# Kernel tuning notes

Hardware: AMD Instinct MI355X
Metric: run time of the kernel (lower is better)

The kernel has to match this reference:

```python
import jax, jax.numpy as jnp
import numpy as np

B, L, D, H = 2, 256, 512, 8
DH = D // H
EPS = 1e-12
NEG = -1000000000000000.0


def setup_inputs() -> dict:
    key = jax.random.key(0)
    ks = jax.random.split(key, 16)
    s = 0.02
    return {
        "inputs": jax.random.normal(ks[0], (B, L, D), jnp.float32),
        "pos_embedding": jax.random.normal(ks[1], (B, L, L, D), jnp.float32),
        "seq_mask": jnp.ones((B, L), jnp.int32),
        "Wq": jax.random.normal(ks[2], (D, D), jnp.float32) * s,
        "bq": jnp.zeros((D,), jnp.float32),
        "Wk": jax.random.normal(ks[3], (D, D), jnp.float32) * s,
        "bk": jnp.zeros((D,), jnp.float32),
        "Wv": jax.random.normal(ks[4], (D, D), jnp.float32) * s,
        "bv": jnp.zeros((D,), jnp.float32),
        "Wr": jax.random.normal(ks[5], (D, D), jnp.float32) * s,
        "br": jnp.zeros((D,), jnp.float32),
        "u": jax.random.normal(ks[6], (H, DH), jnp.float32),
        "v": jax.random.normal(ks[7], (H, DH), jnp.float32),
        "Wf": jax.random.normal(ks[8], (D, D), jnp.float32) * s,
        "bf": jnp.zeros((D,), jnp.float32),
        "gamma": jnp.ones((D,), jnp.float32),
        "beta": jnp.zeros((D,), jnp.float32),
    }


def _layer_norm(x, gamma, beta, eps):
    mu = jnp.mean(x, axis=-1, keepdims=True)
    var = jnp.mean(jnp.square(x - mu), axis=-1, keepdims=True)
    return (x - mu) * jax.lax.rsqrt(var + eps) * gamma + beta


def reference(inputs, pos_embedding, seq_mask, Wq, bq, Wk, bk, Wv, bv, Wr, br,
              u, v, Wf, bf, gamma, beta):
    b, l, d = inputs.shape
    # projections (nn.Linear: x @ W.T + b)
    q = (inputs @ Wq.T + bq).reshape(b, l, H, DH).transpose(0, 2, 1, 3)  # [B,H,L,DH]
    k = (inputs @ Wk.T + bk).reshape(b, l, H, DH).transpose(0, 2, 1, 3)
    vv = (inputs @ Wv.T + bv).reshape(b, l, H, DH).transpose(0, 2, 1, 3)
    rel = (pos_embedding @ Wr.T + br).reshape(b, l, l, H, DH)            # [B,L,L,H,DH]

    # A + C: content-content + content-bias
    A_C = jnp.einsum('bhid,bhjd->bhij', q + u[None, :, None, :], k)
    # B + D: position term against per-(i,j) relative embeddings
    B_D = jnp.einsum('bhid,bijhd->bhij', q + v[None, :, None, :], rel)

    score = (A_C + B_D) / np.sqrt(DH).astype(np.float32)
    invalid = (seq_mask == 0)[:, None, None, :]   # mask keys where seq_mask==0
    score = jnp.where(invalid, NEG, score)
    attn = jax.nn.softmax(score, axis=-1)

    ctx = jnp.einsum('bhij,bhjd->bhid', attn, vv)
    ctx = ctx.transpose(0, 2, 1, 3).reshape(b, l, d)

    # FFN (single dense) + residual + LayerNorm
    h = ctx @ Wf.T + bf
    return _layer_norm(h + inputs, gamma, beta, EPS)
```

## Files before the change

### kernel.cpp

```cpp
#include <hip/hip_runtime.h>
#include <cmath>


typedef __bf16 bf16x8 __attribute__((ext_vector_type(8)));
typedef float f32x4 __attribute__((ext_vector_type(4)));

__device__ __forceinline__ float4 ld4(const float* p) { return *reinterpret_cast<const float4*>(p); }
__device__ __forceinline__ void st4(float* p, float4 v) { *reinterpret_cast<float4*>(p) = v; }
__device__ __forceinline__ void fma4(float4& a, float s, const float4& v) {
    a.x = fmaf(s, v.x, a.x); a.y = fmaf(s, v.y, a.y);
    a.z = fmaf(s, v.z, a.z); a.w = fmaf(s, v.w, a.w);
}
__device__ __forceinline__ float dot4(const float4& a, const float4& b) {
    return a.x*b.x + a.y*b.y + a.z*b.z + a.w*b.w;
}
__device__ __forceinline__ unsigned short f2bf(float f) {
    unsigned int x = __float_as_uint(f);
    unsigned int r = x + 0x7FFFu + ((x >> 16) & 1u);
    return (unsigned short)(r >> 16);
}
__device__ __forceinline__ ushort4 cvt4u(float4 a) {
    ushort4 u;
    u.x = f2bf(a.x); u.y = f2bf(a.y); u.z = f2bf(a.z); u.w = f2bf(a.w);
    return u;
}
__device__ __forceinline__ bf16x8 cvt8(float4 a, float4 b) {
    bf16x8 r;
    r[0] = (__bf16)a.x; r[1] = (__bf16)a.y; r[2] = (__bf16)a.z; r[3] = (__bf16)a.w;
    r[4] = (__bf16)b.x; r[5] = (__bf16)b.y; r[6] = (__bf16)b.z; r[7] = (__bf16)b.w;
    return r;
}

__device__ __forceinline__ void mfma_tile(
        const float* __restrict__ Abase, int ldA,
        const float* __restrict__ Bbase, int ldB,
        int K, int lane, f32x4 acc[4]) {
    int koff = (lane >> 4) * 8;
    int rr = lane & 15;
    const float* ap = Abase + rr * ldA + koff;
    const float* bp = Bbase + rr * ldB + koff;
#pragma unroll 2
    for (int k0 = 0; k0 < K; k0 += 32) {
        float4 a0  = ld4(ap + k0),            a1  = ld4(ap + k0 + 4);
        float4 b00 = ld4(bp + k0),            b01 = ld4(bp + k0 + 4);
        float4 b10 = ld4(bp + 16*ldB + k0),   b11 = ld4(bp + 16*ldB + k0 + 4);
        float4 b20 = ld4(bp + 32*ldB + k0),   b21 = ld4(bp + 32*ldB + k0 + 4);
        float4 b30 = ld4(bp + 48*ldB + k0),   b31 = ld4(bp + 48*ldB + k0 + 4);
        bf16x8 af = cvt8(a0, a1);
        acc[0] = __builtin_amdgcn_mfma_f32_16x16x32_bf16(af, cvt8(b00, b01), acc[0], 0, 0, 0);
        acc[1] = __builtin_amdgcn_mfma_f32_16x16x32_bf16(af, cvt8(b10, b11), acc[1], 0, 0, 0);
        acc[2] = __builtin_amdgcn_mfma_f32_16x16x32_bf16(af, cvt8(b20, b21), acc[2], 0, 0, 0);
        acc[3] = __builtin_amdgcn_mfma_f32_16x16x32_bf16(af, cvt8(b30, b31), acc[3], 0, 0, 0);
    }
}

__global__ __launch_bounds__(256) void k_front(
        const float* __restrict__ x,
        const float* __restrict__ Wq, const float* __restrict__ Wk, const float* __restrict__ Wv,
        const float* __restrict__ bq, const float* __restrict__ bk, const float* __restrict__ bv,
        const float* __restrict__ Wr,
        const float* __restrict__ u, const float* __restrict__ vbv, const float* __restrict__ br,
        float* __restrict__ qw, float* __restrict__ kw, float* __restrict__ vw,
        float* __restrict__ wrt,
        float* __restrict__ c_ws, float* __restrict__ uk_ws, float* __restrict__ vwr_ws) {
    int id = blockIdx.x;
    int t = threadIdx.x;
    if (id < 192) {
        int mat = id >> 6, rem = id & 63;
        int m0 = (rem >> 3) * 64, n0 = (rem & 7) * 64;
        const float* W   = (mat == 0) ? Wq : (mat == 1) ? Wk : Wv;
        const float* bias= (mat == 0) ? bq : (mat == 1) ? bk : bv;
        float* out       = (mat == 0) ? qw : (mat == 1) ? kw : vw;
        int wv = t >> 6, lane = t & 63;
        f32x4 acc[4] = {{0,0,0,0},{0,0,0,0},{0,0,0,0},{0,0,0,0}};
        mfma_tile(x + (m0 + wv * 16) * 512, 512, W + n0 * 512, 512, 512, lane, acc);
        int h = n0 >> 6;
        int col = lane & 15, rbase = (lane >> 4) * 4;
        float rpart[4] = {0, 0, 0, 0};
#pragma unroll
        for (int c = 0; c < 4; c++) {
            int d = c * 16 + col;
            float bv_ = bias[n0 + d];
            float vbd = vbv[n0 + d];
            float brd = br[n0 + d];
            float ud  = u[n0 + d];
#pragma unroll
            for (int r = 0; r < 4; r++) {
                int m = m0 + wv * 16 + rbase + r;
                int b = m >> 8, i = m & 255;
                float val = acc[c][r] + bv_;
                out[((b * 8 + h) * 256 + i) * 64 + d] = val;
                if (mat == 0) rpart[r] += (val + vbd) * brd;
                else if (mat == 1) rpart[r] += val * ud;
            }
        }
        if (mat < 2) {
#pragma unroll
            for (int msk = 1; msk < 16; msk <<= 1) {
#pragma unroll
                for (int r = 0; r < 4; r++) rpart[r] += __shfl_xor(rpart[r], msk, 64);
            }
            if (col == 0) {
                float* dst = (mat == 0) ? c_ws : uk_ws;
#pragma unroll
                for (int r = 0; r < 4; r++) {
                    int m = m0 + wv * 16 + rbase + r;
                    int b = m >> 8, i = m & 255;
                    dst[(b * 8 + h) * 256 + i] = rpart[r];
                }
            }
        }
    } else {
        __shared__ float tile[64][65];
        __shared__ float vpart[4][64];
        int id2 = id - 192;
        int n0 = (id2 >> 3) * 64, k0 = (id2 & 7) * 64;
        int h = n0 >> 6;
        int tx = t & 63, ty = t >> 6;
#pragma unroll
        for (int r = 0; r < 16; r++) {
            int row = ty * 16 + r;
            tile[row][tx] = Wr[(n0 + row) * 512 + k0 + tx];
        }
        __syncthreads();
#pragma unroll
        for (int r = 0; r < 16; r++) {
            int row = ty * 16 + r;
            wrt[(k0 + row) * 512 + n0 + tx] = tile[tx][row];
        }
        float s = 0.f;
#pragma unroll
        for (int r = 0; r < 16; r++) s += vbv[n0 + ty * 16 + r] * tile[ty * 16 + r][tx];
        vpart[ty][tx] = s;
        __syncthreads();
        if (t < 64) vwr_ws[h * 512 + k0 + t] = vpart[0][t] + vpart[1][t] + vpart[2][t] + vpart[3][t];
    }
}

__global__ __launch_bounds__(256) void k_mid(
        const float* __restrict__ qw, const float* __restrict__ kw,
        const float* __restrict__ wrt,
        const float* __restrict__ c_ws, const float* __restrict__ uk_ws,
        const float* __restrict__ vwr_ws,
        float* __restrict__ w_ws, float* __restrict__ ac_ws) {
    int id = blockIdx.x;
    int t = threadIdx.x, wv = t >> 6, lane = t & 63;
    int col = lane & 15, rbase = (lane >> 4) * 4;
    if (id < 512) {
        int h = id >> 6, rem = id & 63;
        int m0 = (rem >> 3) * 64, n0 = (rem & 7) * 64;
        int b = m0 >> 8, i0 = m0 & 255;
        f32x4 acc[4] = {{0,0,0,0},{0,0,0,0},{0,0,0,0},{0,0,0,0}};
        mfma_tile(qw + ((b * 8 + h) * 256 + i0 + wv * 16) * 64, 64,
                  wrt + (size_t)n0 * 512 + h * 64, 512, 64, lane, acc);
#pragma unroll
        for (int c = 0; c < 4; c++) {
            int n = n0 + c * 16 + col;
            float vw_ = vwr_ws[h * 512 + n];
#pragma unroll
            for (int r = 0; r < 4; r++) {
                int m = m0 + wv * 16 + rbase + r;
                w_ws[((size_t)m * 8 + h) * 512 + n] = acc[c][r] + vw_;
            }
        }
    } else {
        int id2 = id - 512;
        int bh = id2 >> 4, rem2 = id2 & 15;
        int b = bh >> 3, h = bh & 7;
        int i0 = (rem2 >> 2) * 64, j0 = (rem2 & 3) * 64;
        f32x4 acc[4] = {{0,0,0,0},{0,0,0,0},{0,0,0,0},{0,0,0,0}};
        mfma_tile(qw + ((b * 8 + h) * 256 + i0 + wv * 16) * 64, 64,
                  kw + ((b * 8 + h) * 256 + j0) * 64, 64, 64, lane, acc);
#pragma unroll
        for (int c = 0; c < 4; c++) {
            int j = j0 + c * 16 + col;
            float ukv = uk_ws[(b * 8 + h) * 256 + j];
#pragma unroll
            for (int r = 0; r < 4; r++) {
                int ii = i0 + wv * 16 + rbase + r;
                float ci = c_ws[(b * 8 + h) * 256 + ii];
                ac_ws[((size_t)(b * 256 + ii) * 8 + h) * 256 + j] = acc[c][r] + ukv + ci;
            }
        }
    }
}

__global__ __launch_bounds__(512, 4) void k_attn(
        const float* __restrict__ pos, const float* __restrict__ w_ws,
        const float* __restrict__ ac_ws, const float* __restrict__ vw,
        const int* __restrict__ seq_mask, float* __restrict__ ctx) {
    int bi = blockIdx.x;
    int b = bi >> 8, i = bi & 255;
    int t = threadIdx.x;
    int wv = t >> 6, lane = t & 63;
    __shared__ unsigned short wl[16 * 512];
    __shared__ float sc[8][256];
    __shared__ unsigned short stage[8][2048];

    {
        int h = t >> 6;
        int j = t & 63;
        const float* src = w_ws + ((size_t)bi * 8 + h) * 512 + j * 8;
        float4 a = ld4(src);
        float4 c = ld4(src + 4);
        char* dst = reinterpret_cast<char*>(wl) + (j >> 2) * 1024 + ((j & 3) * 16 + h) * 16;
        *reinterpret_cast<ushort4*>(dst)     = cvt4u(a);
        *reinterpret_cast<ushort4*>(dst + 8) = cvt4u(c);
    }
    __syncthreads();

    const float* pb = pos + (size_t)bi * (256 * 512);
    int jbase = wv * 32;
    char* sb = reinterpret_cast<char*>(&stage[wv][0]);
    int arow = lane & 15;
    int a_off = arow * 256 + (lane >> 4) * 16;
    int b_off = (lane & 15) * 16 + (lane >> 4) * 256;
    const char* wlc = reinterpret_cast<const char*>(wl);

#pragma unroll
    for (int jt = 0; jt < 2; jt++) {
        f32x4 acc = {0, 0, 0, 0};
#pragma unroll
        for (int eh = 0; eh < 4; eh++) {
            const float* src = pb + (size_t)(jbase + jt * 16 + (lane >> 5)) * 512
                             + eh * 128 + (lane & 31) * 4;
            float4 tmp[8];
#pragma unroll
            for (int s = 0; s < 8; s++) tmp[s] = ld4(src + (size_t)s * 2 * 512);
#pragma unroll
            for (int s = 0; s < 8; s++) {
                int row = (lane >> 5) + s * 2;
                *reinterpret_cast<ushort4*>(sb + row * 256 + (lane & 31) * 8) = cvt4u(tmp[s]);
            }
#pragma unroll
            for (int es = 0; es < 4; es++) {
                bf16x8 af = *reinterpret_cast<const bf16x8*>(sb + a_off + es * 64);
                int estep = eh * 4 + es;
                bf16x8 bf = *reinterpret_cast<const bf16x8*>(wlc + estep * 1024 + b_off);
                acc = __builtin_amdgcn_mfma_f32_16x16x32_bf16(af, bf, acc, 0, 0, 0);
            }
        }
        int h = lane & 15;
        int rbase = (lane >> 4) * 4;
        if (h < 8) {
#pragma unroll
            for (int r = 0; r < 4; r++) sc[h][jbase + jt * 16 + rbase + r] = acc[r];
        }
    }
    __syncthreads();

    {
        int h = wv;
        const float* acrow = ac_ws + ((b * 256 + i) * 8 + h) * 256;
        float vals[4];
        float mx = -INFINITY;
#pragma unroll
        for (int r = 0; r < 4; r++) {
            int j = lane + r * 64;
            float s = (sc[h][j] + acrow[j]) * 0.125f;
            if (seq_mask[b * 256 + j] == 0) s = -1e15f;
            vals[r] = s;
            mx = fmaxf(mx, s);
        }
#pragma unroll
        for (int m = 32; m >= 1; m >>= 1) mx = fmaxf(mx, __shfl_xor(mx, m, 64));
        float sum = 0.f;
#pragma unroll
        for (int r = 0; r < 4; r++) { vals[r] = __expf(vals[r] - mx); sum += vals[r]; }
#pragma unroll
        for (int m = 32; m >= 1; m >>= 1) sum += __shfl_xor(sum, m, 64);
        float inv = 1.0f / sum;
#pragma unroll
        for (int r = 0; r < 4; r++) sc[h][lane + r * 64] = vals[r] * inv;
    }

    float4* part = reinterpret_cast<float4*>(&stage[0][0]);
    {
        int h = wv;
        int d4 = (lane & 15) * 4;
        int js = lane >> 4;
        const float* vbase = vw + (size_t)(b * 8 + h) * 256 * 64 + d4;
        float4 acc = {0, 0, 0, 0};
#pragma unroll 2
        for (int r = 0; r < 64; r += 4) {
            int j = js * 64 + r;
            float p0 = sc[h][j + 0], p1 = sc[h][j + 1];
            float p2 = sc[h][j + 2], p3 = sc[h][j + 3];
            float4 v0 = ld4(vbase + (size_t)(j + 0) * 64);
            float4 v1 = ld4(vbase + (size_t)(j + 1) * 64);
            float4 v2 = ld4(vbase + (size_t)(j + 2) * 64);
            float4 v3 = ld4(vbase + (size_t)(j + 3) * 64);
            fma4(acc, p0, v0); fma4(acc, p1, v1);
            fma4(acc, p2, v2); fma4(acc, p3, v3);
        }
        part[(h * 4 + js) * 16 + (lane & 15)] = acc;
    }
    {
        int h = wv;
        if ((lane >> 4) == 0) {
            int l = lane & 15;
            float4 a0 = part[(h * 4 + 0) * 16 + l], a1 = part[(h * 4 + 1) * 16 + l];
            float4 a2 = part[(h * 4 + 2) * 16 + l], a3 = part[(h * 4 + 3) * 16 + l];
            float4 o;
            o.x = a0.x + a1.x + a2.x + a3.x;
            o.y = a0.y + a1.y + a2.y + a3.y;
            o.z = a0.z + a1.z + a2.z + a3.z;
            o.w = a0.w + a1.w + a2.w + a3.w;
            st4(ctx + (size_t)(b * 256 + i) * 512 + h * 64 + l * 4, o);
        }
    }
}

__global__ __launch_bounds__(256) void k_ffn(
        const float* __restrict__ A, const float* __restrict__ Wf,
        const float* __restrict__ bias, const float* __restrict__ resid,
        float* __restrict__ outp) {
    int m0 = blockIdx.x * 64, n0 = blockIdx.y * 64;
    int t = threadIdx.x, wv = t >> 6, lane = t & 63;
    f32x4 acc[4] = {{0,0,0,0},{0,0,0,0},{0,0,0,0},{0,0,0,0}};
    mfma_tile(A + (m0 + wv * 16) * 512, 512, Wf + n0 * 512, 512, 512, lane, acc);
    int col = lane & 15, rbase = (lane >> 4) * 4;
#pragma unroll
    for (int c = 0; c < 4; c++) {
        int n = n0 + c * 16 + col;
        float bv_ = bias[n];
#pragma unroll
        for (int r = 0; r < 4; r++) {
            int m = m0 + wv * 16 + rbase + r;
            outp[m * 512 + n] = acc[c][r] + bv_ + resid[m * 512 + n];
        }
    }
}

__global__ __launch_bounds__(256) void k_ln(
        const float* __restrict__ tmp, const float* __restrict__ gamma,
        const float* __restrict__ beta, float* __restrict__ out) {
    int m = blockIdx.x, t = threadIdx.x;
    int wv = t >> 6, lane = t & 63;
    float2 xv = *reinterpret_cast<const float2*>(&tmp[m * 512 + t * 2]);
    __shared__ float red[4];
    float s = xv.x + xv.y;
#pragma unroll
    for (int k = 32; k >= 1; k >>= 1) s += __shfl_xor(s, k, 64);
    if (lane == 0) red[wv] = s;
    __syncthreads();
    float mu = (red[0] + red[1] + red[2] + red[3]) * (1.0f / 512.0f);
    __syncthreads();
    float dx = xv.x - mu, dy = xv.y - mu;
    float vs = dx * dx + dy * dy;
#pragma unroll
    for (int k = 32; k >= 1; k >>= 1) vs += __shfl_xor(vs, k, 64);
    if (lane == 0) red[wv] = vs;
    __syncthreads();
    float var = (red[0] + red[1] + red[2] + red[3]) * (1.0f / 512.0f);
    float rstd = rsqrtf(var + 1e-12f);
    float2 g = *reinterpret_cast<const float2*>(&gamma[t * 2]);
    float2 be = *reinterpret_cast<const float2*>(&beta[t * 2]);
    float2 o;
    o.x = dx * rstd * g.x + be.x;
    o.y = dy * rstd * g.y + be.y;
    *reinterpret_cast<float2*>(&out[m * 512 + t * 2]) = o;
}

extern "C" void kernel_launch(void* const* d_in, const int* in_sizes, int n_in,
                              void* d_out, int out_size, void* d_ws, size_t ws_size,
                              hipStream_t stream) {
    const float* x     = (const float*)d_in[0];
    const float* pos   = (const float*)d_in[1];
    const int*   smask = (const int*)d_in[2];
    const float* Wq = (const float*)d_in[3];
    const float* bq = (const float*)d_in[4];
    const float* Wk = (const float*)d_in[5];
    const float* bk = (const float*)d_in[6];
    const float* Wv = (const float*)d_in[7];
    const float* bv = (const float*)d_in[8];
    const float* Wr = (const float*)d_in[9];
    const float* br = (const float*)d_in[10];
    const float* u  = (const float*)d_in[11];
    const float* vb = (const float*)d_in[12];
    const float* Wf = (const float*)d_in[13];
    const float* bf = (const float*)d_in[14];
    const float* gamma = (const float*)d_in[15];
    const float* beta  = (const float*)d_in[16];
    float* out = (float*)d_out;

    float* ws = (float*)d_ws;
    float* q_ws   = ws;
    float* k_ws   = q_ws  + 262144;
    float* v_ws   = k_ws  + 262144;
    float* w_ws   = v_ws  + 262144;
    float* ac_ws  = w_ws  + 2097152;
    float* ctx_ws = ac_ws + 1048576;
    float* tmp_ws = ctx_ws + 262144;
    float* wrt_ws = tmp_ws + 262144;
    float* c_ws   = wrt_ws + 262144;
    float* uk_ws  = c_ws  + 4096;
    float* vwr_ws = uk_ws + 4096;

    k_front<<<dim3(256), 256, 0, stream>>>(x, Wq, Wk, Wv, bq, bk, bv, Wr, u, vb, br,
                                           q_ws, k_ws, v_ws, wrt_ws, c_ws, uk_ws, vwr_ws);
    k_mid<<<dim3(768), 256, 0, stream>>>(q_ws, k_ws, wrt_ws, c_ws, uk_ws, vwr_ws, w_ws, ac_ws);
    k_attn<<<dim3(512), 512, 0, stream>>>(pos, w_ws, ac_ws, v_ws, smask, ctx_ws);
    k_ffn<<<dim3(8, 8), 256, 0, stream>>>(ctx_ws, Wf, bf, x, tmp_ws);
    k_ln<<<dim3(512), 256, 0, stream>>>(tmp_ws, gamma, beta, out);
}
```

Measured before the change: 108.1 us.

## Fuse output projection, residual and LayerNorm into attention kernel epilogue

```diff
diff --git a/kernel.cpp b/kernel.cpp
--- a/kernel.cpp
+++ b/kernel.cpp
@@ -58,10 +58,10 @@
         const float* __restrict__ x,
         const float* __restrict__ Wq, const float* __restrict__ Wk, const float* __restrict__ Wv,
         const float* __restrict__ bq, const float* __restrict__ bk, const float* __restrict__ bv,
-        const float* __restrict__ Wr,
+        const float* __restrict__ Wr, const float* __restrict__ Wf,
         const float* __restrict__ u, const float* __restrict__ vbv, const float* __restrict__ br,
         float* __restrict__ qw, float* __restrict__ kw, float* __restrict__ vw,
-        float* __restrict__ wrt,
+        float* __restrict__ wrt, float* __restrict__ wft,
         float* __restrict__ c_ws, float* __restrict__ uk_ws, float* __restrict__ vwr_ws) {
     int id = blockIdx.x;
     int t = threadIdx.x;
@@ -113,27 +113,32 @@
     } else {
         __shared__ float tile[64][65];
         __shared__ float vpart[4][64];
-        int id2 = id - 192;
+        int isWf = (id >= 256);
+        int id2 = id - (isWf ? 256 : 192);
+        const float* Wsrc = isWf ? Wf : Wr;
+        float* Wdst = isWf ? wft : wrt;
         int n0 = (id2 >> 3) * 64, k0 = (id2 & 7) * 64;
         int h = n0 >> 6;
         int tx = t & 63, ty = t >> 6;
 #pragma unroll
         for (int r = 0; r < 16; r++) {
             int row = ty * 16 + r;
-            tile[row][tx] = Wr[(n0 + row) * 512 + k0 + tx];
+            tile[row][tx] = Wsrc[(n0 + row) * 512 + k0 + tx];
         }
         __syncthreads();
 #pragma unroll
         for (int r = 0; r < 16; r++) {
             int row = ty * 16 + r;
-            wrt[(k0 + row) * 512 + n0 + tx] = tile[tx][row];
-        }
-        float s = 0.f;
-#pragma unroll
-        for (int r = 0; r < 16; r++) s += vbv[n0 + ty * 16 + r] * tile[ty * 16 + r][tx];
-        vpart[ty][tx] = s;
-        __syncthreads();
-        if (t < 64) vwr_ws[h * 512 + k0 + t] = vpart[0][t] + vpart[1][t] + vpart[2][t] + vpart[3][t];
+            Wdst[(k0 + row) * 512 + n0 + tx] = tile[tx][row];
+        }
+        if (!isWf) {
+            float s = 0.f;
+#pragma unroll
+            for (int r = 0; r < 16; r++) s += vbv[n0 + ty * 16 + r] * tile[ty * 16 + r][tx];
+            vpart[ty][tx] = s;
+            __syncthreads();
+            if (t < 64) vwr_ws[h * 512 + k0 + t] = vpart[0][t] + vpart[1][t] + vpart[2][t] + vpart[3][t];
+        }
     }
 }
 
@@ -188,7 +193,11 @@
 __global__ __launch_bounds__(512, 4) void k_attn(
         const float* __restrict__ pos, const float* __restrict__ w_ws,
         const float* __restrict__ ac_ws, const float* __restrict__ vw,
-        const int* __restrict__ seq_mask, float* __restrict__ ctx) {
+        const int* __restrict__ seq_mask,
+        const float* __restrict__ wft, const float* __restrict__ bf,
+        const float* __restrict__ x,
+        const float* __restrict__ gamma, const float* __restrict__ beta,
+        float* __restrict__ outp) {
     int bi = blockIdx.x;
     int b = bi >> 8, i = bi & 255;
     int t = threadIdx.x;
@@ -196,6 +205,8 @@
     __shared__ unsigned short wl[16 * 512];
     __shared__ float sc[8][256];
     __shared__ unsigned short stage[8][2048];
+    __shared__ float ctxl[512];
+    __shared__ float lnred[8][2];
 
     {
         int h = t >> 6;
@@ -236,8 +247,8 @@
             for (int es = 0; es < 4; es++) {
                 bf16x8 af = *reinterpret_cast<const bf16x8*>(sb + a_off + es * 64);
                 int estep = eh * 4 + es;
-                bf16x8 bf = *reinterpret_cast<const bf16x8*>(wlc + estep * 1024 + b_off);
-                acc = __builtin_amdgcn_mfma_f32_16x16x32_bf16(af, bf, acc, 0, 0, 0);
+                bf16x8 bf_ = *reinterpret_cast<const bf16x8*>(wlc + estep * 1024 + b_off);
+                acc = __builtin_amdgcn_mfma_f32_16x16x32_bf16(af, bf_, acc, 0, 0, 0);
             }
         }
         int h = lane & 15;
@@ -306,60 +317,45 @@
             o.y = a0.y + a1.y + a2.y + a3.y;
             o.z = a0.z + a1.z + a2.z + a3.z;
             o.w = a0.w + a1.w + a2.w + a3.w;
-            st4(ctx + (size_t)(b * 256 + i) * 512 + h * 64 + l * 4, o);
-        }
-    }
-}
-
-__global__ __launch_bounds__(256) void k_ffn(
-        const float* __restrict__ A, const float* __restrict__ Wf,
-        const float* __restrict__ bias, const float* __restrict__ resid,
-        float* __restrict__ outp) {
-    int m0 = blockIdx.x * 64, n0 = blockIdx.y * 64;
-    int t = threadIdx.x, wv = t >> 6, lane = t & 63;
-    f32x4 acc[4] = {{0,0,0,0},{0,0,0,0},{0,0,0,0},{0,0,0,0}};
-    mfma_tile(A + (m0 + wv * 16) * 512, 512, Wf + n0 * 512, 512, 512, lane, acc);
-    int col = lane & 15, rbase = (lane >> 4) * 4;
-#pragma unroll
-    for (int c = 0; c < 4; c++) {
-        int n = n0 + c * 16 + col;
-        float bv_ = bias[n];
-#pragma unroll
-        for (int r = 0; r < 4; r++) {
-            int m = m0 + wv * 16 + rbase + r;
-            outp[m * 512 + n] = acc[c][r] + bv_ + resid[m * 512 + n];
-        }
-    }
-}
-
-__global__ __launch_bounds__(256) void k_ln(
-        const float* __restrict__ tmp, const float* __restrict__ gamma,
-        const float* __restrict__ beta, float* __restrict__ out) {
-    int m = blockIdx.x, t = threadIdx.x;
-    int wv = t >> 6, lane = t & 63;
-    float2 xv = *reinterpret_cast<const float2*>(&tmp[m * 512 + t * 2]);
-    __shared__ float red[4];
-    float s = xv.x + xv.y;
-#pragma unroll
-    for (int k = 32; k >= 1; k >>= 1) s += __shfl_xor(s, k, 64);
-    if (lane == 0) red[wv] = s;
+            st4(&ctxl[h * 64 + l * 4], o);
+        }
+    }
     __syncthreads();
-    float mu = (red[0] + red[1] + red[2] + red[3]) * (1.0f / 512.0f);
-    __syncthreads();
-    float dx = xv.x - mu, dy = xv.y - mu;
-    float vs = dx * dx + dy * dy;
-#pragma unroll
-    for (int k = 32; k >= 1; k >>= 1) vs += __shfl_xor(vs, k, 64);
-    if (lane == 0) red[wv] = vs;
-    __syncthreads();
-    float var = (red[0] + red[1] + red[2] + red[3]) * (1.0f / 512.0f);
-    float rstd = rsqrtf(var + 1e-12f);
-    float2 g = *reinterpret_cast<const float2*>(&gamma[t * 2]);
-    float2 be = *reinterpret_cast<const float2*>(&beta[t * 2]);
-    float2 o;
-    o.x = dx * rstd * g.x + be.x;
-    o.y = dy * rstd * g.y + be.y;
-    *reinterpret_cast<float2*>(&out[m * 512 + t * 2]) = o;
+
+    {
+        int n = wv * 64 + lane;
+        const float* wcol = wft + n;
+        float acc = 0.f;
+#pragma unroll 4
+        for (int k0 = 0; k0 < 512; k0 += 8) {
+            float4 c0 = ld4(&ctxl[k0]);
+            float4 c1 = ld4(&ctxl[k0 + 4]);
+            acc = fmaf(c0.x, wcol[(size_t)(k0 + 0) * 512], acc);
+            acc = fmaf(c0.y, wcol[(size_t)(k0 + 1) * 512], acc);
+            acc = fmaf(c0.z, wcol[(size_t)(k0 + 2) * 512], acc);
+            acc = fmaf(c0.w, wcol[(size_t)(k0 + 3) * 512], acc);
+            acc = fmaf(c1.x, wcol[(size_t)(k0 + 4) * 512], acc);
+            acc = fmaf(c1.y, wcol[(size_t)(k0 + 5) * 512], acc);
+            acc = fmaf(c1.z, wcol[(size_t)(k0 + 6) * 512], acc);
+            acc = fmaf(c1.w, wcol[(size_t)(k0 + 7) * 512], acc);
+        }
+        float v = acc + bf[n] + x[(size_t)(b * 256 + i) * 512 + n];
+        float s = v, q = v * v;
+#pragma unroll
+        for (int m = 32; m >= 1; m >>= 1) {
+            s += __shfl_xor(s, m, 64);
+            q += __shfl_xor(q, m, 64);
+        }
+        if (lane == 0) { lnred[wv][0] = s; lnred[wv][1] = q; }
+        __syncthreads();
+        float ts = 0.f, tq = 0.f;
+#pragma unroll
+        for (int w2 = 0; w2 < 8; w2++) { ts += lnred[w2][0]; tq += lnred[w2][1]; }
+        float mu = ts * (1.0f / 512.0f);
+        float var = tq * (1.0f / 512.0f) - mu * mu;
+        float rstd = rsqrtf(var + 1e-12f);
+        outp[(size_t)(b * 256 + i) * 512 + n] = (v - mu) * rstd * gamma[n] + beta[n];
+    }
 }
 
 extern "C" void kernel_launch(void* const* d_in, const int* in_sizes, int n_in,
@@ -390,17 +386,16 @@
     float* v_ws   = k_ws  + 262144;
     float* w_ws   = v_ws  + 262144;
     float* ac_ws  = w_ws  + 2097152;
-    float* ctx_ws = ac_ws + 1048576;
-    float* tmp_ws = ctx_ws + 262144;
-    float* wrt_ws = tmp_ws + 262144;
-    float* c_ws   = wrt_ws + 262144;
+    float* wrt_ws = ac_ws + 1048576;
+    float* wft_ws = wrt_ws + 262144;
+    float* c_ws   = wft_ws + 262144;
     float* uk_ws  = c_ws  + 4096;
     float* vwr_ws = uk_ws + 4096;
 
-    k_front<<<dim3(256), 256, 0, stream>>>(x, Wq, Wk, Wv, bq, bk, bv, Wr, u, vb, br,
-                                           q_ws, k_ws, v_ws, wrt_ws, c_ws, uk_ws, vwr_ws);
+    k_front<<<dim3(320), 256, 0, stream>>>(x, Wq, Wk, Wv, bq, bk, bv, Wr, Wf, u, vb, br,
+                                           q_ws, k_ws, v_ws, wrt_ws, wft_ws,
+                                           c_ws, uk_ws, vwr_ws);
     k_mid<<<dim3(768), 256, 0, stream>>>(q_ws, k_ws, wrt_ws, c_ws, uk_ws, vwr_ws, w_ws, ac_ws);
-    k_attn<<<dim3(512), 512, 0, stream>>>(pos, w_ws, ac_ws, v_ws, smask, ctx_ws);
-    k_ffn<<<dim3(8, 8), 256, 0, stream>>>(ctx_ws, Wf, bf, x, tmp_ws);
-    k_ln<<<dim3(512), 256, 0, stream>>>(tmp_ws, gamma, beta, out);
-}
+    k_attn<<<dim3(512), 512, 0, stream>>>(pos, w_ws, ac_ws, v_ws, smask,
+                                          wft_ws, bf, x, gamma, beta, out);
+}
```

Result: faster. 103.4 us, median of 2 (-4.4%).
